# Kernel tuning notes

Hardware: AMD Instinct MI355X
Metric: run time of the kernel (lower is better)

The kernel has to match this reference:

```python
import jax, jax.numpy as jnp
import numpy as np

R = 16
ALPHA = 32
SCALING = ALPHA / R  # 2.0
IN_F = 4096
OUT_F = 4096

def setup_inputs() -> dict:
    key = jax.random.key(0)
    k1, k2, k3, k4 = jax.random.split(key, 4)
    x = jax.random.normal(k1, (4, 2048, IN_F), dtype=jnp.float32)
    # kaiming_uniform init for lora_A in torch; randn is fine for a numeric baseline
    lora_A = jax.random.normal(k2, (R, IN_F), dtype=jnp.float32) * 0.02
    lora_B = jax.random.normal(k3, (OUT_F, R), dtype=jnp.float32) * 0.02
    bias = jax.random.normal(k4, (OUT_F,), dtype=jnp.float32) * 0.01
    return {"x": x, "lora_A": lora_A, "lora_B": lora_B, "bias": bias}

def reference(x, lora_A, lora_B, bias):
    # Faithful to torch: W = lora_B @ lora_A * scaling ([out, in]), then x @ W^T + bias
    W = (lora_B @ lora_A) * SCALING            # [out, in]
    out = jnp.einsum('bsi,oi->bso', x, W) + bias  # [B, S, out]
    return out
```

## Files before the change

kernel.cpp:

```cpp
#include <hip/hip_runtime.h>
#include <hip/hip_bf16.h>
#include <stdint.h>


constexpr int IN_F  = 4096;
constexpr int OUT_F = 4096;
constexpr int RANK  = 16;
constexpr int M_TOT = 4 * 2048;
constexpr float SCALING = 2.0f;

typedef const __attribute__((address_space(1))) void* as1_cvp;
typedef __attribute__((address_space(3))) void*       as3_vp;

__global__ __launch_bounds__(256, 4) void lora_phase1(
    const float* __restrict__ x, const float* __restrict__ A,
    float* __restrict__ t)
{
    __shared__ float4 As[2][RANK][64];
    const int lane = threadIdx.x & 63;
    const int wave = threadIdx.x >> 6;
    const int row0 = blockIdx.x * 8 + wave * 2;

    const float4* __restrict__ A4 = (const float4*)A;
    const float4* __restrict__ x0 = (const float4*)(x + (size_t)row0 * IN_F);
    const float4* __restrict__ x1 = (const float4*)(x + (size_t)(row0 + 1) * IN_F);

    float acc0[RANK], acc1[RANK];
#pragma unroll
    for (int r = 0; r < RANK; ++r) { acc0[r] = 0.0f; acc1[r] = 0.0f; }

#pragma unroll
    for (int rr = 0; rr < 4; ++rr) {
        const int r = wave * 4 + rr;
        __builtin_amdgcn_global_load_lds((as1_cvp)(A4 + (size_t)r * (IN_F / 4) + lane),
                                         (as3_vp)(&As[0][r][0]), 16, 0, 0);
    }
    float4 xc0 = x0[lane];
    float4 xc1 = x1[lane];
    __syncthreads();

    int buf = 0;
#pragma unroll 1
    for (int j = 0; j < 16; ++j) {
        float4 xn0, xn1;
        if (j < 15) {
            const int c4 = (j + 1) * 64 + lane;
#pragma unroll
            for (int rr = 0; rr < 4; ++rr) {
                const int r = wave * 4 + rr;
                __builtin_amdgcn_global_load_lds(
                    (as1_cvp)(A4 + (size_t)r * (IN_F / 4) + c4),
                    (as3_vp)(&As[buf ^ 1][r][0]), 16, 0, 0);
            }
            xn0 = x0[c4];
            xn1 = x1[c4];
        }

#pragma unroll
        for (int r = 0; r < RANK; ++r) {
            const float4 av = As[buf][r][lane];
            acc0[r] += xc0.x * av.x;
            acc0[r] += xc0.y * av.y;
            acc0[r] += xc0.z * av.z;
            acc0[r] += xc0.w * av.w;
            acc1[r] += xc1.x * av.x;
            acc1[r] += xc1.y * av.y;
            acc1[r] += xc1.z * av.z;
            acc1[r] += xc1.w * av.w;
        }

        if (j < 15) {
            __syncthreads();
            buf ^= 1;
            xc0 = xn0;
            xc1 = xn1;
        }
    }

#pragma unroll
    for (int p = 0; p < 2; ++p) {
        float out_v = 0.0f;
#pragma unroll
        for (int r = 0; r < RANK; ++r) {
            float v = (p == 0) ? acc0[r] : acc1[r];
#pragma unroll
            for (int s = 1; s < 64; s <<= 1)
                v += __shfl_xor(v, s, 64);
            out_v = (lane == r) ? v : out_v;
        }
        if (lane < RANK)
            t[(size_t)(row0 + p) * RANK + lane] = SCALING * out_v;
    }
}

__global__ __launch_bounds__(256) void lora_phase2(
    const float* __restrict__ t, const float* __restrict__ B,
    const float* __restrict__ bias, float* __restrict__ out)
{
    const int o0 = blockIdx.x * 1024 + threadIdx.x * 4;
    const int m0 = blockIdx.y * 4;

    const float4* __restrict__ B4 = (const float4*)B;
    const float4* __restrict__ t4 = (const float4*)t;

    float4 b[4][4];
#pragma unroll
    for (int q = 0; q < 4; ++q)
#pragma unroll
        for (int rr = 0; rr < 4; ++rr)
            b[q][rr] = B4[(size_t)(o0 + q) * 4 + rr];

    float4 tv[4][4];
#pragma unroll
    for (int mi = 0; mi < 4; ++mi)
#pragma unroll
        for (int rr = 0; rr < 4; ++rr)
            tv[mi][rr] = t4[(size_t)(m0 + mi) * 4 + rr];

    const float4 bs = *(const float4*)(bias + o0);

#pragma unroll
    for (int mi = 0; mi < 4; ++mi) {
        float v[4] = {bs.x, bs.y, bs.z, bs.w};
#pragma unroll
        for (int q = 0; q < 4; ++q) {
#pragma unroll
            for (int rr = 0; rr < 4; ++rr) {
                v[q] += b[q][rr].x * tv[mi][rr].x;
                v[q] += b[q][rr].y * tv[mi][rr].y;
                v[q] += b[q][rr].z * tv[mi][rr].z;
                v[q] += b[q][rr].w * tv[mi][rr].w;
            }
        }
        float4 o4 = {v[0], v[1], v[2], v[3]};
        *(float4*)(out + (size_t)(m0 + mi) * OUT_F + o0) = o4;
    }
}

extern "C" void kernel_launch(void* const* d_in, const int* in_sizes, int n_in,
                              void* d_out, int out_size, void* d_ws, size_t ws_size,
                              hipStream_t stream) {
    const float* x    = (const float*)d_in[0];
    const float* A    = (const float*)d_in[1];
    const float* B    = (const float*)d_in[2];
    const float* bias = (const float*)d_in[3];
    float* out = (float*)d_out;
    float* t   = (float*)d_ws;

    lora_phase1<<<dim3(M_TOT / 8), dim3(256), 0, stream>>>(x, A, t);
    lora_phase2<<<dim3(OUT_F / 1024, M_TOT / 4), dim3(256), 0, stream>>>(t, B, bias, out);
}
```

Measured before the change: 295.8 us.

## Fuse LoRA down and up projections into one kernel with LDS intermediate

```diff
diff --git a/kernel.cpp b/kernel.cpp
--- a/kernel.cpp
+++ b/kernel.cpp
@@ -1,5 +1,4 @@
 #include <hip/hip_runtime.h>
-#include <hip/hip_bf16.h>
 #include <stdint.h>
 
 
@@ -11,19 +10,24 @@
 
 typedef const __attribute__((address_space(1))) void* as1_cvp;
 typedef __attribute__((address_space(3))) void*       as3_vp;
+typedef float f32x4 __attribute__((ext_vector_type(4)));
 
-__global__ __launch_bounds__(256, 4) void lora_phase1(
+__global__ __launch_bounds__(256, 4) void lora_fused(
     const float* __restrict__ x, const float* __restrict__ A,
-    float* __restrict__ t)
+    const float* __restrict__ B, const float* __restrict__ bias,
+    float* __restrict__ out)
 {
     __shared__ float4 As[2][RANK][64];
+    __shared__ float  t_lds[8][RANK];
+
     const int lane = threadIdx.x & 63;
     const int wave = threadIdx.x >> 6;
-    const int row0 = blockIdx.x * 8 + wave * 2;
+    const int mblk = blockIdx.x * 8;
+    const int row0 = mblk + wave * 2;
 
     const float4* __restrict__ A4 = (const float4*)A;
-    const float4* __restrict__ x0 = (const float4*)(x + (size_t)row0 * IN_F);
-    const float4* __restrict__ x1 = (const float4*)(x + (size_t)(row0 + 1) * IN_F);
+    const f32x4*  __restrict__ x0 = (const f32x4*)(x + (size_t)row0 * IN_F);
+    const f32x4*  __restrict__ x1 = (const f32x4*)(x + (size_t)(row0 + 1) * IN_F);
 
     float acc0[RANK], acc1[RANK];
 #pragma unroll
@@ -35,14 +39,14 @@
         __builtin_amdgcn_global_load_lds((as1_cvp)(A4 + (size_t)r * (IN_F / 4) + lane),
                                          (as3_vp)(&As[0][r][0]), 16, 0, 0);
     }
-    float4 xc0 = x0[lane];
-    float4 xc1 = x1[lane];
+    f32x4 xc0 = __builtin_nontemporal_load(x0 + lane);
+    f32x4 xc1 = __builtin_nontemporal_load(x1 + lane);
     __syncthreads();
 
     int buf = 0;
 #pragma unroll 1
     for (int j = 0; j < 16; ++j) {
-        float4 xn0, xn1;
+        f32x4 xn0, xn1;
         if (j < 15) {
             const int c4 = (j + 1) * 64 + lane;
 #pragma unroll
@@ -52,8 +56,8 @@
                     (as1_cvp)(A4 + (size_t)r * (IN_F / 4) + c4),
                     (as3_vp)(&As[buf ^ 1][r][0]), 16, 0, 0);
             }
-            xn0 = x0[c4];
-            xn1 = x1[c4];
+            xn0 = __builtin_nontemporal_load(x0 + c4);
+            xn1 = __builtin_nontemporal_load(x1 + c4);
         }
 
 #pragma unroll
@@ -89,51 +93,47 @@
             out_v = (lane == r) ? v : out_v;
         }
         if (lane < RANK)
-            t[(size_t)(row0 + p) * RANK + lane] = SCALING * out_v;
+            t_lds[wave * 2 + p][lane] = SCALING * out_v;
     }
-}
-
-__global__ __launch_bounds__(256) void lora_phase2(
-    const float* __restrict__ t, const float* __restrict__ B,
-    const float* __restrict__ bias, float* __restrict__ out)
-{
-    const int o0 = blockIdx.x * 1024 + threadIdx.x * 4;
-    const int m0 = blockIdx.y * 4;
+    __syncthreads();
 
     const float4* __restrict__ B4 = (const float4*)B;
-    const float4* __restrict__ t4 = (const float4*)t;
+#pragma unroll 1
+    for (int c = 0; c < 4; ++c) {
+        const int o0 = c * 1024 + threadIdx.x * 4;
 
-    float4 b[4][4];
+        float4 b[4][4];
 #pragma unroll
-    for (int q = 0; q < 4; ++q)
+        for (int q = 0; q < 4; ++q)
 #pragma unroll
-        for (int rr = 0; rr < 4; ++rr)
-            b[q][rr] = B4[(size_t)(o0 + q) * 4 + rr];
+            for (int rr = 0; rr < 4; ++rr)
+                b[q][rr] = B4[(size_t)(o0 + q) * 4 + rr];
 
-    float4 tv[4][4];
-#pragma unroll
-    for (int mi = 0; mi < 4; ++mi)
-#pragma unroll
-        for (int rr = 0; rr < 4; ++rr)
-            tv[mi][rr] = t4[(size_t)(m0 + mi) * 4 + rr];
-
-    const float4 bs = *(const float4*)(bias + o0);
+        const float4 bs = *(const float4*)(bias + o0);
 
 #pragma unroll
-    for (int mi = 0; mi < 4; ++mi) {
-        float v[4] = {bs.x, bs.y, bs.z, bs.w};
+        for (int mi = 0; mi < 8; ++mi) {
+            const float4 tv0 = *(const float4*)&t_lds[mi][0];
+            const float4 tv1 = *(const float4*)&t_lds[mi][4];
+            const float4 tv2 = *(const float4*)&t_lds[mi][8];
+            const float4 tv3 = *(const float4*)&t_lds[mi][12];
+            const float4 tv[4] = {tv0, tv1, tv2, tv3};
+
+            float v[4] = {bs.x, bs.y, bs.z, bs.w};
 #pragma unroll
-        for (int q = 0; q < 4; ++q) {
+            for (int q = 0; q < 4; ++q) {
 #pragma unroll
-            for (int rr = 0; rr < 4; ++rr) {
-                v[q] += b[q][rr].x * tv[mi][rr].x;
-                v[q] += b[q][rr].y * tv[mi][rr].y;
-                v[q] += b[q][rr].z * tv[mi][rr].z;
-                v[q] += b[q][rr].w * tv[mi][rr].w;
+                for (int rr = 0; rr < 4; ++rr) {
+                    v[q] += b[q][rr].x * tv[rr].x;
+                    v[q] += b[q][rr].y * tv[rr].y;
+                    v[q] += b[q][rr].z * tv[rr].z;
+                    v[q] += b[q][rr].w * tv[rr].w;
+                }
             }
+            f32x4 o4 = {v[0], v[1], v[2], v[3]};
+            __builtin_nontemporal_store(
+                o4, (f32x4*)(out + (size_t)(mblk + mi) * OUT_F + o0));
         }
-        float4 o4 = {v[0], v[1], v[2], v[3]};
-        *(float4*)(out + (size_t)(m0 + mi) * OUT_F + o0) = o4;
     }
 }
 
@@ -145,8 +145,7 @@
     const float* B    = (const float*)d_in[2];
     const float* bias = (const float*)d_in[3];
     float* out = (float*)d_out;
-    float* t   = (float*)d_ws;
+    (void)d_ws; (void)ws_size;
 
-    lora_phase1<<<dim3(M_TOT / 8), dim3(256), 0, stream>>>(x, A, t);
-    lora_phase2<<<dim3(OUT_F / 1024, M_TOT / 4), dim3(256), 0, stream>>>(t, B, bias, out);
+    lora_fused<<<dim3(M_TOT / 8), dim3(256), 0, stream>>>(x, A, B, bias, out);
 }
```

Result: slower. 442.6 us (+49.6%).

## Transpose lora_B for coalesced phase-2 loads and enlarge phase-1 blocks

Applied to the files above, without the earlier changes.

```diff
diff --git a/kernel.cpp b/kernel.cpp
--- a/kernel.cpp
+++ b/kernel.cpp
@@ -1,5 +1,4 @@
 #include <hip/hip_runtime.h>
-#include <hip/hip_bf16.h>
 #include <stdint.h>
 
 
@@ -11,15 +10,16 @@
 
 typedef const __attribute__((address_space(1))) void* as1_cvp;
 typedef __attribute__((address_space(3))) void*       as3_vp;
-
-__global__ __launch_bounds__(256, 4) void lora_phase1(
+typedef float f32x4 __attribute__((ext_vector_type(4)));
+
+__global__ __launch_bounds__(512, 4) void lora_phase1(
     const float* __restrict__ x, const float* __restrict__ A,
     float* __restrict__ t)
 {
     __shared__ float4 As[2][RANK][64];
     const int lane = threadIdx.x & 63;
     const int wave = threadIdx.x >> 6;
-    const int row0 = blockIdx.x * 8 + wave * 2;
+    const int row0 = blockIdx.x * 16 + wave * 2;
 
     const float4* __restrict__ A4 = (const float4*)A;
     const float4* __restrict__ x0 = (const float4*)(x + (size_t)row0 * IN_F);
@@ -30,8 +30,8 @@
     for (int r = 0; r < RANK; ++r) { acc0[r] = 0.0f; acc1[r] = 0.0f; }
 
 #pragma unroll
-    for (int rr = 0; rr < 4; ++rr) {
-        const int r = wave * 4 + rr;
+    for (int rr = 0; rr < 2; ++rr) {
+        const int r = wave * 2 + rr;
         __builtin_amdgcn_global_load_lds((as1_cvp)(A4 + (size_t)r * (IN_F / 4) + lane),
                                          (as3_vp)(&As[0][r][0]), 16, 0, 0);
     }
@@ -46,8 +46,8 @@
         if (j < 15) {
             const int c4 = (j + 1) * 64 + lane;
 #pragma unroll
-            for (int rr = 0; rr < 4; ++rr) {
-                const int r = wave * 4 + rr;
+            for (int rr = 0; rr < 2; ++rr) {
+                const int r = wave * 2 + rr;
                 __builtin_amdgcn_global_load_lds(
                     (as1_cvp)(A4 + (size_t)r * (IN_F / 4) + c4),
                     (as3_vp)(&As[buf ^ 1][r][0]), 16, 0, 0);
@@ -93,6 +93,57 @@
     }
 }
 
+__global__ __launch_bounds__(256) void transpose_B(
+    const float* __restrict__ B, float* __restrict__ BT)
+{
+    const int id = blockIdx.x * 256 + threadIdx.x;
+    const float4 v = ((const float4*)B)[id];
+    const int o = id >> 2;
+    const int k = id & 3;
+    BT[(size_t)(4 * k + 0) * OUT_F + o] = v.x;
+    BT[(size_t)(4 * k + 1) * OUT_F + o] = v.y;
+    BT[(size_t)(4 * k + 2) * OUT_F + o] = v.z;
+    BT[(size_t)(4 * k + 3) * OUT_F + o] = v.w;
+}
+
+__global__ __launch_bounds__(256) void lora_phase2t(
+    const float* __restrict__ t, const float* __restrict__ BT,
+    const float* __restrict__ bias, float* __restrict__ out)
+{
+    const int o0 = blockIdx.x * 1024 + threadIdx.x * 4;
+    const int m0 = blockIdx.y * 4;
+
+    const f32x4* __restrict__ BT4 = (const f32x4*)BT;
+    const float4* __restrict__ t4 = (const float4*)t;
+
+    f32x4 b[16];
+#pragma unroll
+    for (int r = 0; r < 16; ++r)
+        b[r] = BT4[(size_t)r * (OUT_F / 4) + (o0 >> 2)];
+
+    float4 tv[4][4];
+#pragma unroll
+    for (int mi = 0; mi < 4; ++mi)
+#pragma unroll
+        for (int rr = 0; rr < 4; ++rr)
+            tv[mi][rr] = t4[(size_t)(m0 + mi) * 4 + rr];
+
+    const f32x4 bs = *(const f32x4*)(bias + o0);
+
+#pragma unroll
+    for (int mi = 0; mi < 4; ++mi) {
+        f32x4 v = bs;
+#pragma unroll
+        for (int rr = 0; rr < 4; ++rr) {
+            v += b[4 * rr + 0] * tv[mi][rr].x;
+            v += b[4 * rr + 1] * tv[mi][rr].y;
+            v += b[4 * rr + 2] * tv[mi][rr].z;
+            v += b[4 * rr + 3] * tv[mi][rr].w;
+        }
+        *(f32x4*)(out + (size_t)(m0 + mi) * OUT_F + o0) = v;
+    }
+}
+
 __global__ __launch_bounds__(256) void lora_phase2(
     const float* __restrict__ t, const float* __restrict__ B,
     const float* __restrict__ bias, float* __restrict__ out)
@@ -147,6 +198,17 @@
     float* out = (float*)d_out;
     float* t   = (float*)d_ws;
 
-    lora_phase1<<<dim3(M_TOT / 8), dim3(256), 0, stream>>>(x, A, t);
-    lora_phase2<<<dim3(OUT_F / 1024, M_TOT / 4), dim3(256), 0, stream>>>(t, B, bias, out);
-}
+    const size_t need_bt = (size_t)(M_TOT * RANK + RANK * OUT_F) * sizeof(float);
+    const bool use_bt = ws_size >= need_bt;
+    float* BT = t + (size_t)M_TOT * RANK;
+
+    if (use_bt)
+        transpose_B<<<dim3(64), dim3(256), 0, stream>>>(B, BT);
+
+    lora_phase1<<<dim3(M_TOT / 16), dim3(512), 0, stream>>>(x, A, t);
+
+    if (use_bt)
+        lora_phase2t<<<dim3(OUT_F / 1024, M_TOT / 4), dim3(256), 0, stream>>>(t, BT, bias, out);
+    else
+        lora_phase2<<<dim3(OUT_F / 1024, M_TOT / 4), dim3(256), 0, stream>>>(t, B, bias, out);
+}
```

Measured after the change: 262.4 us. 1.13x faster.
